# Optimization experiments

Hardware: AMD Instinct MI355X
Metric: run time of the kernel (lower is better)

Reference implementation:

```python
import jax, jax.numpy as jnp
import numpy as np

N, E, IN, ED, H = 50000, 500000, 27, 12, 128
LAYERS = 3


def _bn(h, g, b):
    # BatchNorm1d, training-mode batch statistics, biased variance, eps=1e-5
    mu = h.mean(0)
    var = h.var(0)
    return (h - mu) * jax.lax.rsqrt(var + 1e-5) * g + b


def _layer(x, src, dst, ea, eps, eW, eb, W1, b1, g1, be1, W2, b2, ng, nb):
    # GINEConv: project edge_attr to node dim, message = relu(x_j + e), sum-aggregate
    e = ea @ eW + eb                                   # [E, in_dim]
    m = jax.nn.relu(x[src] + e)                        # [E, in_dim]
    agg = jax.ops.segment_sum(m, dst, num_segments=N)  # [N, in_dim]
    h = (1.0 + eps) * x + agg
    # conv MLP: Linear -> BN -> ReLU -> (Dropout eval=id) -> Linear
    h = jax.nn.relu(_bn(h @ W1 + b1, g1, be1))
    h = h @ W2 + b2
    # outer BatchNorm -> ReLU -> (Dropout eval=id)
    return jax.nn.relu(_bn(h, ng, nb))


def setup_inputs() -> dict:
    key = jax.random.key(0)
    ks = iter(jax.random.split(key, 64))
    d = {}
    d["x"] = jax.random.normal(next(ks), (N, IN), jnp.float32)
    d["edge_index"] = jax.random.randint(next(ks), (2, E), 0, N, jnp.int32)
    d["edge_attr"] = jax.random.normal(next(ks), (E, ED), jnp.float32)
    for i in range(LAYERS):
        ind = IN if i == 0 else H
        d[f"l{i}_eps"] = jnp.zeros((), jnp.float32)
        d[f"l{i}_eW"] = jax.random.normal(next(ks), (ED, ind), jnp.float32) * 0.1
        d[f"l{i}_eb"] = jnp.zeros((ind,), jnp.float32)
        d[f"l{i}_W1"] = jax.random.normal(next(ks), (ind, 2 * H), jnp.float32) * (1.0 / np.sqrt(ind))
        d[f"l{i}_b1"] = jnp.zeros((2 * H,), jnp.float32)
        d[f"l{i}_g1"] = jnp.ones((2 * H,), jnp.float32)
        d[f"l{i}_be1"] = jnp.zeros((2 * H,), jnp.float32)
        d[f"l{i}_W2"] = jax.random.normal(next(ks), (2 * H, H), jnp.float32) * (1.0 / np.sqrt(2 * H))
        d[f"l{i}_b2"] = jnp.zeros((H,), jnp.float32)
        d[f"l{i}_ng"] = jnp.ones((H,), jnp.float32)
        d[f"l{i}_nb"] = jnp.zeros((H,), jnp.float32)
    return d


def reference(x, edge_index, edge_attr,
              l0_eps, l0_eW, l0_eb, l0_W1, l0_b1, l0_g1, l0_be1, l0_W2, l0_b2, l0_ng, l0_nb,
              l1_eps, l1_eW, l1_eb, l1_W1, l1_b1, l1_g1, l1_be1, l1_W2, l1_b2, l1_ng, l1_nb,
              l2_eps, l2_eW, l2_eb, l2_W1, l2_b1, l2_g1, l2_be1, l2_W2, l2_b2, l2_ng, l2_nb):
    src, dst = edge_index[0], edge_index[1]
    P = [
        (l0_eps, l0_eW, l0_eb, l0_W1, l0_b1, l0_g1, l0_be1, l0_W2, l0_b2, l0_ng, l0_nb),
        (l1_eps, l1_eW, l1_eb, l1_W1, l1_b1, l1_g1, l1_be1, l1_W2, l1_b2, l1_ng, l1_nb),
        (l2_eps, l2_eW, l2_eb, l2_W1, l2_b1, l2_g1, l2_be1, l2_W2, l2_b2, l2_ng, l2_nb),
    ]
    h = x
    for i, p in enumerate(P):
        out = _layer(h, src, dst, edge_attr, *p)
        if 0 < i < LAYERS - 1 and out.shape == h.shape:
            h = h + 0.3 * out
        else:
            h = out
    return h
```

## Files before the change

### kernel.cpp

```cpp
#include <hip/hip_runtime.h>
#include <hip/hip_bf16.h>


typedef __attribute__((ext_vector_type(8))) short bf16x8;
typedef __attribute__((ext_vector_type(4))) float f32x4;

static inline int cdiv(int a, int b) { return (a + b - 1) / b; }

__device__ inline ushort f2bf(float f) {
    uint32_t u = __float_as_uint(f);
    return (ushort)((u + 0x7FFFu + ((u >> 16) & 1u)) >> 16);
}
__device__ inline float bf2f(ushort h) { return __uint_as_float(((uint32_t)h) << 16); }

__global__ __launch_bounds__(256) void histogram_dst(const int* __restrict__ dst,
                                                     int* __restrict__ deg, int E) {
    int i = blockIdx.x * blockDim.x + threadIdx.x;
    int stride = gridDim.x * blockDim.x;
    for (; i < E; i += stride) atomicAdd(&deg[dst[i]], 1);
}

__global__ __launch_bounds__(1024) void scan_deg(const int* __restrict__ deg,
                                                 int* __restrict__ rowptr, int N) {
    __shared__ int part[1024];
    int t = threadIdx.x;
    int chunk = (N + 1023) / 1024;
    int b = t * chunk;
    int e = b + chunk;
    if (b > N) b = N;
    if (e > N) e = N;
    int s = 0;
    for (int i = b; i < e; ++i) s += deg[i];
    part[t] = s;
    __syncthreads();
    for (int off = 1; off < 1024; off <<= 1) {
        int v = (t >= off) ? part[t - off] : 0;
        __syncthreads();
        part[t] += v;
        __syncthreads();
    }
    int base = (t == 0) ? 0 : part[t - 1];
    for (int i = b; i < e; ++i) {
        rowptr[i] = base;
        base += deg[i];
    }
    if (t == 1023) rowptr[N] = base;
}

__global__ __launch_bounds__(256) void scatter_edges(const int* __restrict__ dst,
                                                     int* __restrict__ cursor,
                                                     int* __restrict__ eid, int E) {
    int i = blockIdx.x * blockDim.x + threadIdx.x;
    int stride = gridDim.x * blockDim.x;
    for (; i < E; i += stride) {
        int pos = atomicAdd(&cursor[dst[i]], 1);
        eid[pos] = i;
    }
}

__global__ __launch_bounds__(256) void gather128(
    const int* __restrict__ rowptr, const int* __restrict__ eid, const int* __restrict__ src,
    const float* __restrict__ ea, const float* __restrict__ eW, const float* __restrict__ eb,
    const float* __restrict__ x, const float* __restrict__ epsp, float* __restrict__ agg, int N) {
    __shared__ __align__(16) float sW[12 * 128];
    __shared__ __align__(16) float sb[128];
    int tid = threadIdx.x;
    for (int i = tid; i < 12 * 128; i += 256) sW[i] = eW[i];
    if (tid < 128) sb[tid] = eb[tid];
    __syncthreads();

    float onePlusEps = 1.0f + *epsp;
    int lane = tid & 31;
    int n = blockIdx.x * 8 + (tid >> 5);
    if (n >= N) return;
    int beg = rowptr[n], end = rowptr[n + 1];
    int d0 = lane << 2;
    float4 bb = *(const float4*)&sb[d0];
    float4 acc = make_float4(0.f, 0.f, 0.f, 0.f);

    int i = beg;
    for (; i + 4 <= end; i += 4) {
        int e[4], s[4];
        float av[4];
        float4 xv[4], p[4];
#pragma unroll
        for (int j = 0; j < 4; ++j) e[j] = eid[i + j];
#pragma unroll
        for (int j = 0; j < 4; ++j) {
            s[j] = src[e[j]];
            av[j] = (lane < 12) ? ea[(size_t)e[j] * 12 + lane] : 0.0f;
        }
#pragma unroll
        for (int j = 0; j < 4; ++j) {
            xv[j] = *(const float4*)&x[(size_t)s[j] * 128 + d0];
            p[j] = bb;
        }
#pragma unroll
        for (int k = 0; k < 12; ++k) {
            float4 w = *(const float4*)&sW[k * 128 + d0];
#pragma unroll
            for (int j = 0; j < 4; ++j) {
                float a = __shfl(av[j], k, 32);
                p[j].x = fmaf(a, w.x, p[j].x);
                p[j].y = fmaf(a, w.y, p[j].y);
                p[j].z = fmaf(a, w.z, p[j].z);
                p[j].w = fmaf(a, w.w, p[j].w);
            }
        }
#pragma unroll
        for (int j = 0; j < 4; ++j) {
            acc.x += fmaxf(xv[j].x + p[j].x, 0.f);
            acc.y += fmaxf(xv[j].y + p[j].y, 0.f);
            acc.z += fmaxf(xv[j].z + p[j].z, 0.f);
            acc.w += fmaxf(xv[j].w + p[j].w, 0.f);
        }
    }
    for (; i < end; ++i) {
        int e = eid[i];
        int s = src[e];
        float av = (lane < 12) ? ea[(size_t)e * 12 + lane] : 0.0f;
        float4 p = bb;
#pragma unroll
        for (int k = 0; k < 12; ++k) {
            float ak = __shfl(av, k, 32);
            float4 w = *(const float4*)&sW[k * 128 + d0];
            p.x = fmaf(ak, w.x, p.x);
            p.y = fmaf(ak, w.y, p.y);
            p.z = fmaf(ak, w.z, p.z);
            p.w = fmaf(ak, w.w, p.w);
        }
        float4 xv = *(const float4*)&x[(size_t)s * 128 + d0];
        acc.x += fmaxf(xv.x + p.x, 0.f);
        acc.y += fmaxf(xv.y + p.y, 0.f);
        acc.z += fmaxf(xv.z + p.z, 0.f);
        acc.w += fmaxf(xv.w + p.w, 0.f);
    }
    float4 xn = *(const float4*)&x[(size_t)n * 128 + d0];
    float4 o;
    o.x = fmaf(onePlusEps, xn.x, acc.x);
    o.y = fmaf(onePlusEps, xn.y, acc.y);
    o.z = fmaf(onePlusEps, xn.z, acc.z);
    o.w = fmaf(onePlusEps, xn.w, acc.w);
    *(float4*)&agg[(size_t)n * 128 + d0] = o;
}

__global__ __launch_bounds__(256) void gather27(
    const int* __restrict__ rowptr, const int* __restrict__ eid, const int* __restrict__ src,
    const float* __restrict__ ea, const float* __restrict__ eW, const float* __restrict__ eb,
    const float* __restrict__ x, const float* __restrict__ epsp, float* __restrict__ agg, int N) {
    __shared__ __align__(16) float sW[12 * 28 + 4];
    __shared__ __align__(16) float sb[32];
    int tid = threadIdx.x;
    for (int i = tid; i < 12 * 28 + 4; i += 256) sW[i] = 0.0f;
    if (tid < 32) sb[tid] = 0.0f;
    __syncthreads();
    for (int i = tid; i < 12 * 27; i += 256) {
        int k = i / 27, d = i - k * 27;
        sW[k * 28 + d] = eW[i];
    }
    if (tid < 27) sb[tid] = eb[tid];
    __syncthreads();

    float onePlusEps = 1.0f + *epsp;
    int lane = tid & 31;
    int n = blockIdx.x * 8 + (tid >> 5);
    if (n >= N) return;
    int beg = rowptr[n], end = rowptr[n + 1];
    int sub = lane >> 3, sl = lane & 7;
    int d0 = sl << 2;
    int d0c = (sl < 7) ? d0 : 24;
    float4 bb = *(const float4*)&sb[d0c];
    float4 acc = make_float4(0.f, 0.f, 0.f, 0.f);

    int iters = (end - beg + 3) >> 2;
    for (int it = 0; it < iters; ++it) {
        int i = beg + it * 4 + sub;
        bool v = i < end;
        int e = v ? eid[i] : 0;
        int s = v ? src[e] : 0;
        float avA = v ? ea[(size_t)e * 12 + sl] : 0.0f;
        float avB = (v && sl < 4) ? ea[(size_t)e * 12 + 8 + sl] : 0.0f;
        float4 xv = make_float4(0.f, 0.f, 0.f, 0.f);
        if (v) {
            if (sl < 6) {
                xv = *(const float4*)&x[(size_t)s * 27 + d0];
            } else if (sl == 6) {
                xv.x = x[(size_t)s * 27 + 24];
                xv.y = x[(size_t)s * 27 + 25];
                xv.z = x[(size_t)s * 27 + 26];
            }
        }
        float4 p = bb;
#pragma unroll
        for (int k = 0; k < 8; ++k) {
            float ak = __shfl(avA, k, 8);
            float4 w = *(const float4*)&sW[k * 28 + d0c];
            p.x = fmaf(ak, w.x, p.x);
            p.y = fmaf(ak, w.y, p.y);
            p.z = fmaf(ak, w.z, p.z);
            p.w = fmaf(ak, w.w, p.w);
        }
#pragma unroll
        for (int k = 8; k < 12; ++k) {
            float ak = __shfl(avB, k - 8, 8);
            float4 w = *(const float4*)&sW[k * 28 + d0c];
            p.x = fmaf(ak, w.x, p.x);
            p.y = fmaf(ak, w.y, p.y);
            p.z = fmaf(ak, w.z, p.z);
            p.w = fmaf(ak, w.w, p.w);
        }
        if (v) {
            acc.x += fmaxf(xv.x + p.x, 0.f);
            acc.y += fmaxf(xv.y + p.y, 0.f);
            acc.z += fmaxf(xv.z + p.z, 0.f);
            acc.w += fmaxf(xv.w + p.w, 0.f);
        }
    }
    acc.x += __shfl_xor(acc.x, 8, 32);
    acc.y += __shfl_xor(acc.y, 8, 32);
    acc.z += __shfl_xor(acc.z, 8, 32);
    acc.w += __shfl_xor(acc.w, 8, 32);
    acc.x += __shfl_xor(acc.x, 16, 32);
    acc.y += __shfl_xor(acc.y, 16, 32);
    acc.z += __shfl_xor(acc.z, 16, 32);
    acc.w += __shfl_xor(acc.w, 16, 32);

    if (sub == 0) {
        if (sl < 6) {
            float4 xn = *(const float4*)&x[(size_t)n * 27 + d0];
            float4 o;
            o.x = fmaf(onePlusEps, xn.x, acc.x);
            o.y = fmaf(onePlusEps, xn.y, acc.y);
            o.z = fmaf(onePlusEps, xn.z, acc.z);
            o.w = fmaf(onePlusEps, xn.w, acc.w);
            *(float4*)&agg[(size_t)n * 27 + d0] = o;
        } else if (sl == 6) {
            agg[(size_t)n * 27 + 24] = fmaf(onePlusEps, x[(size_t)n * 27 + 24], acc.x);
            agg[(size_t)n * 27 + 25] = fmaf(onePlusEps, x[(size_t)n * 27 + 25], acc.y);
            agg[(size_t)n * 27 + 26] = fmaf(onePlusEps, x[(size_t)n * 27 + 26], acc.z);
        }
    }
}

__global__ __launch_bounds__(256) void repack_w(const float* __restrict__ W, int K, int N,
                                                ushort* __restrict__ hi, ushort* __restrict__ lo) {
    int kg = (K + 31) / 32;
    int total = (N / 16) * kg * 64;
    int idx = blockIdx.x * 256 + threadIdx.x;
    if (idx >= total) return;
    int l = idx & 63;
    int g = (idx >> 6) % kg;
    int t = (idx >> 6) / kg;
#pragma unroll
    for (int j = 0; j < 8; ++j) {
        int k = g * 32 + ((l >> 4) << 3) + j;
        int n = (t << 4) + (l & 15);
        float v = (k < K) ? W[(size_t)k * N + n] : 0.0f;
        ushort h = f2bf(v);
        hi[(size_t)idx * 8 + j] = h;
        lo[(size_t)idx * 8 + j] = f2bf(v - bf2f(h));
    }
}

template <int NF, bool PRE_BN>
__global__ __launch_bounds__(512) void mfma_gemm(const float* __restrict__ A, int M, int K,
                                                 const ushort* __restrict__ Wph,
                                                 const ushort* __restrict__ Wpl,
                                                 const float* __restrict__ bias,
                                                 const float* __restrict__ scale,
                                                 const float* __restrict__ shift,
                                                 float* __restrict__ C, int ldc,
                                                 float* __restrict__ sums,
                                                 float* __restrict__ sumsq) {
    __shared__ __align__(16) ushort As_hi[128 * 32];
    __shared__ __align__(16) ushort As_lo[128 * 32];
    int tid = threadIdx.x;
    int lane = tid & 63;
    int wv = tid >> 6;
    int wm = wv >> 2, wn = wv & 3;
    int row0 = blockIdx.x * 128;
    int kg = (K + 31) >> 5;

    f32x4 acc[4][NF] = {};

    for (int g = 0; g < kg; ++g) {
        int k0 = g << 5;
        for (int c = tid; c < 1024; c += 512) {
            int row = c >> 3;
            int kc = (c & 7) << 2;
            int gm = row0 + row;
            float v[4] = {0.f, 0.f, 0.f, 0.f};
            if (gm < M) {
                const float* ap = &A[(size_t)gm * K + k0 + kc];
                if (k0 + kc + 4 <= K) {
                    float4 t4 = *(const float4*)ap;
                    v[0] = t4.x; v[1] = t4.y; v[2] = t4.z; v[3] = t4.w;
                } else {
#pragma unroll
                    for (int t = 0; t < 4; ++t)
                        if (k0 + kc + t < K) v[t] = ap[t];
                }
                if (PRE_BN) {
#pragma unroll
                    for (int t = 0; t < 4; ++t) {
                        int k = k0 + kc + t;
                        if (k < K) v[t] = fmaxf(fmaf(v[t], scale[k], shift[k]), 0.0f);
                    }
                }
            }
            ushort h[4], l2[4];
#pragma unroll
            for (int t = 0; t < 4; ++t) {
                h[t] = f2bf(v[t]);
                l2[t] = f2bf(v[t] - bf2f(h[t]));
            }
            int e = row * 32 + kc;
            *(ushort4*)&As_hi[e] = make_ushort4(h[0], h[1], h[2], h[3]);
            *(ushort4*)&As_lo[e] = make_ushort4(l2[0], l2[1], l2[2], l2[3]);
        }
        __syncthreads();

        bf16x8 ah[4], al[4];
#pragma unroll
        for (int mf = 0; mf < 4; ++mf) {
            int e = ((wm << 6) + (mf << 4) + (lane & 15)) * 32 + ((lane >> 4) << 3);
            ah[mf] = *(const bf16x8*)&As_hi[e];
            al[mf] = *(const bf16x8*)&As_lo[e];
        }
#pragma unroll
        for (int nf = 0; nf < NF; ++nf) {
            int tn = wn * NF + nf;
            size_t off = (((size_t)tn * kg + g) * 64 + lane) * 8;
            bf16x8 bh = *(const bf16x8*)(Wph + off);
            bf16x8 bl = *(const bf16x8*)(Wpl + off);
#pragma unroll
            for (int mf = 0; mf < 4; ++mf) {
                acc[mf][nf] =
                    __builtin_amdgcn_mfma_f32_16x16x32_bf16(ah[mf], bh, acc[mf][nf], 0, 0, 0);
                acc[mf][nf] =
                    __builtin_amdgcn_mfma_f32_16x16x32_bf16(ah[mf], bl, acc[mf][nf], 0, 0, 0);
                acc[mf][nf] =
                    __builtin_amdgcn_mfma_f32_16x16x32_bf16(al[mf], bh, acc[mf][nf], 0, 0, 0);
            }
        }
        __syncthreads();
    }

#pragma unroll
    for (int nf = 0; nf < NF; ++nf) {
        int col = (wn * NF + nf) * 16 + (lane & 15);
        float bv = bias[col];
        float s = 0.f, qs = 0.f;
#pragma unroll
        for (int mf = 0; mf < 4; ++mf) {
            int rbase = row0 + (wm << 6) + (mf << 4) + ((lane >> 4) << 2);
#pragma unroll
            for (int q = 0; q < 4; ++q) {
                int row = rbase + q;
                if (row < M) {
                    float v = acc[mf][nf][q] + bv;
                    C[(size_t)row * ldc + col] = v;
                    s += v;
                    qs = fmaf(v, v, qs);
                }
            }
        }
        s += __shfl_xor(s, 16);
        s += __shfl_xor(s, 32);
        qs += __shfl_xor(qs, 16);
        qs += __shfl_xor(qs, 32);
        if (lane < 16) {
            atomicAdd(&sums[col], s);
            atomicAdd(&sumsq[col], qs);
        }
    }
}

__global__ void finalize_bn(const float* __restrict__ sums, const float* __restrict__ sumsq,
                            const float* __restrict__ g, const float* __restrict__ b,
                            float* __restrict__ scale, float* __restrict__ shift, int C,
                            float invN) {
    int c = blockIdx.x * blockDim.x + threadIdx.x;
    if (c < C) {
        float mu = sums[c] * invN;
        float var = sumsq[c] * invN - mu * mu;
        float inv = rsqrtf(var + 1e-5f);
        float sc = g[c] * inv;
        scale[c] = sc;
        shift[c] = b[c] - mu * sc;
    }
}

template <bool RES>
__global__ __launch_bounds__(256) void bn_apply(const float* __restrict__ h,
                                                const float* __restrict__ scale,
                                                const float* __restrict__ shift,
                                                const float* __restrict__ xprev,
                                                float* __restrict__ out, int total4) {
    int i = blockIdx.x * blockDim.x + threadIdx.x;
    int stride = gridDim.x * blockDim.x;
    for (; i < total4; i += stride) {
        int c0 = (i & 31) << 2;
        float4 v = ((const float4*)h)[i];
        float4 o;
        o.x = fmaxf(fmaf(v.x, scale[c0 + 0], shift[c0 + 0]), 0.0f);
        o.y = fmaxf(fmaf(v.y, scale[c0 + 1], shift[c0 + 1]), 0.0f);
        o.z = fmaxf(fmaf(v.z, scale[c0 + 2], shift[c0 + 2]), 0.0f);
        o.w = fmaxf(fmaf(v.w, scale[c0 + 3], shift[c0 + 3]), 0.0f);
        if (RES) {
            float4 xp = ((const float4*)xprev)[i];
            o.x = fmaf(0.3f, o.x, xp.x);
            o.y = fmaf(0.3f, o.y, xp.y);
            o.z = fmaf(0.3f, o.z, xp.z);
            o.w = fmaf(0.3f, o.w, xp.w);
        }
        ((float4*)out)[i] = o;
    }
}

extern "C" void kernel_launch(void* const* d_in, const int* in_sizes, int n_in, void* d_out,
                              int out_size, void* d_ws, size_t ws_size, hipStream_t stream) {
    const float* x_in = (const float*)d_in[0];
    const int* ei = (const int*)d_in[1];
    const float* ea = (const float*)d_in[2];
    const int IN_DIM = 27;
    const int H = 128;
    int N = in_sizes[0] / IN_DIM;
    int E = in_sizes[1] / 2;
    const int* src = ei;
    const int* dst = ei + E;

    auto L = [&](int layer, int j) -> const float* {
        return (const float*)d_in[3 + 11 * layer + j];
    };

    float* X0 = (float*)d_ws;
    float* AGG = X0 + (size_t)N * H;
    float* H1 = AGG + (size_t)N * H;
    float* STATS = H1 + (size_t)N * 2 * H;
    float* sums1 = STATS;
    float* sq1 = STATS + 256;
    float* sums2 = STATS + 512;
    float* sq2 = STATS + 640;
    float* scale1 = STATS + 768;
    float* shift1 = STATS + 1024;
    float* scale2 = STATS + 1280;
    float* shift2 = STATS + 1408;
    int* rowptr = (int*)(STATS + 1536);
    int* cursor = rowptr + (N + 1);
    int* eid = cursor + N;
    size_t wp_off = ((size_t)(eid + E - (int*)d_ws) * 4 + 15) & ~(size_t)15;
    ushort* Wp1h = (ushort*)((char*)d_ws + wp_off);
    ushort* Wp1l = Wp1h + 32768;
    ushort* Wp2h = Wp1l + 32768;
    ushort* Wp2l = Wp2h + 32768;
    float* X1 = (float*)d_out;

    float invN = 1.0f / (float)N;
    int gridM = cdiv(N, 128);
    int gatherG = cdiv(N, 8);

    hipMemsetAsync(rowptr, 0, (size_t)(N + 1) * sizeof(int), stream);
    histogram_dst<<<1024, 256, 0, stream>>>(dst, rowptr, E);
    scan_deg<<<1, 1024, 0, stream>>>(rowptr, cursor, N);
    hipMemcpyAsync(rowptr, cursor, (size_t)(N + 1) * sizeof(int), hipMemcpyDeviceToDevice, stream);
    scatter_edges<<<1024, 256, 0, stream>>>(dst, cursor, eid, E);

    for (int i = 0; i < 3; ++i) {
        int ind = (i == 0) ? IN_DIM : H;
        const float* xin = (i == 0) ? x_in : ((i == 1) ? X0 : X1);
        float* xout = (i == 2) ? (float*)d_out : ((i == 0) ? X0 : X1);

        hipMemsetAsync(STATS, 0, 768 * sizeof(float), stream);

        int kg1 = cdiv(ind, 32);
        int tot1 = 16 * kg1 * 64;
        repack_w<<<cdiv(tot1, 256), 256, 0, stream>>>(L(i, 3), ind, 256, Wp1h, Wp1l);
        int tot2 = 8 * 8 * 64;
        repack_w<<<cdiv(tot2, 256), 256, 0, stream>>>(L(i, 7), 256, 128, Wp2h, Wp2l);

        if (i == 0)
            gather27<<<gatherG, 256, 0, stream>>>(rowptr, eid, src, ea, L(i, 1), L(i, 2), xin,
                                                  L(i, 0), AGG, N);
        else
            gather128<<<gatherG, 256, 0, stream>>>(rowptr, eid, src, ea, L(i, 1), L(i, 2), xin,
                                                   L(i, 0), AGG, N);

        mfma_gemm<4, false><<<gridM, 512, 0, stream>>>(AGG, N, ind, Wp1h, Wp1l, L(i, 4), nullptr,
                                                       nullptr, H1, 256, sums1, sq1);
        finalize_bn<<<1, 256, 0, stream>>>(sums1, sq1, L(i, 5), L(i, 6), scale1, shift1, 256, invN);

        mfma_gemm<2, true><<<gridM, 512, 0, stream>>>(H1, N, 256, Wp2h, Wp2l, L(i, 8), scale1,
                                                      shift1, AGG, 128, sums2, sq2);
        finalize_bn<<<1, 256, 0, stream>>>(sums2, sq2, L(i, 9), L(i, 10), scale2, shift2, 128,
                                           invN);

        int total4 = N * H / 4;
        if (i == 1)
            bn_apply<true><<<2048, 256, 0, stream>>>(AGG, scale2, shift2, X0, xout, total4);
        else
            bn_apply<false><<<2048, 256, 0, stream>>>(AGG, scale2, shift2, nullptr, xout, total4);
    }
}
```

Measured before the change: 821.1 us.

## Batch weight repacks, fold BN finalize into consumers, pad LDS, predicate gather tail

```diff
diff --git a/kernel.cpp b/kernel.cpp
--- a/kernel.cpp
+++ b/kernel.cpp
@@ -78,13 +78,17 @@
     float4 bb = *(const float4*)&sb[d0];
     float4 acc = make_float4(0.f, 0.f, 0.f, 0.f);
 
-    int i = beg;
-    for (; i + 4 <= end; i += 4) {
+    int iters = (end - beg + 3) >> 2;
+    for (int it = 0; it < iters; ++it) {
+        int i = beg + it * 4;
         int e[4], s[4];
         float av[4];
         float4 xv[4], p[4];
 #pragma unroll
-        for (int j = 0; j < 4; ++j) e[j] = eid[i + j];
+        for (int j = 0; j < 4; ++j) {
+            int idx = i + j;
+            e[j] = eid[(idx < end) ? idx : i];
+        }
 #pragma unroll
         for (int j = 0; j < 4; ++j) {
             s[j] = src[e[j]];
@@ -109,31 +113,12 @@
         }
 #pragma unroll
         for (int j = 0; j < 4; ++j) {
-            acc.x += fmaxf(xv[j].x + p[j].x, 0.f);
-            acc.y += fmaxf(xv[j].y + p[j].y, 0.f);
-            acc.z += fmaxf(xv[j].z + p[j].z, 0.f);
-            acc.w += fmaxf(xv[j].w + p[j].w, 0.f);
-        }
-    }
-    for (; i < end; ++i) {
-        int e = eid[i];
-        int s = src[e];
-        float av = (lane < 12) ? ea[(size_t)e * 12 + lane] : 0.0f;
-        float4 p = bb;
-#pragma unroll
-        for (int k = 0; k < 12; ++k) {
-            float ak = __shfl(av, k, 32);
-            float4 w = *(const float4*)&sW[k * 128 + d0];
-            p.x = fmaf(ak, w.x, p.x);
-            p.y = fmaf(ak, w.y, p.y);
-            p.z = fmaf(ak, w.z, p.z);
-            p.w = fmaf(ak, w.w, p.w);
-        }
-        float4 xv = *(const float4*)&x[(size_t)s * 128 + d0];
-        acc.x += fmaxf(xv.x + p.x, 0.f);
-        acc.y += fmaxf(xv.y + p.y, 0.f);
-        acc.z += fmaxf(xv.z + p.z, 0.f);
-        acc.w += fmaxf(xv.w + p.w, 0.f);
+            bool v = (i + j) < end;
+            acc.x += v ? fmaxf(xv[j].x + p[j].x, 0.f) : 0.f;
+            acc.y += v ? fmaxf(xv[j].y + p[j].y, 0.f) : 0.f;
+            acc.z += v ? fmaxf(xv[j].z + p[j].z, 0.f) : 0.f;
+            acc.w += v ? fmaxf(xv[j].w + p[j].w, 0.f) : 0.f;
+        }
     }
     float4 xn = *(const float4*)&x[(size_t)n * 128 + d0];
     float4 o;
@@ -242,20 +227,34 @@
     }
 }
 
-__global__ __launch_bounds__(256) void repack_w(const float* __restrict__ W, int K, int N,
-                                                ushort* __restrict__ hi, ushort* __restrict__ lo) {
-    int kg = (K + 31) / 32;
-    int total = (N / 16) * kg * 64;
+__global__ __launch_bounds__(256) void repack_all(const float* __restrict__ w0,
+                                                  const float* __restrict__ w1,
+                                                  const float* __restrict__ w2,
+                                                  const float* __restrict__ w3,
+                                                  const float* __restrict__ w4,
+                                                  const float* __restrict__ w5,
+                                                  ushort* __restrict__ hi,
+                                                  ushort* __restrict__ lo) {
     int idx = blockIdx.x * 256 + threadIdx.x;
-    if (idx >= total) return;
-    int l = idx & 63;
-    int g = (idx >> 6) % kg;
-    int t = (idx >> 6) / kg;
+    if (idx >= 21504) return;
+    const float* W;
+    int base, K, NC;
+    if (idx < 1024)       { W = w0; base = 0;     K = 27;  NC = 256; }
+    else if (idx < 5120)  { W = w1; base = 1024;  K = 256; NC = 128; }
+    else if (idx < 9216)  { W = w2; base = 5120;  K = 128; NC = 256; }
+    else if (idx < 13312) { W = w3; base = 9216;  K = 256; NC = 128; }
+    else if (idx < 17408) { W = w4; base = 13312; K = 128; NC = 256; }
+    else                  { W = w5; base = 17408; K = 256; NC = 128; }
+    int li = idx - base;
+    int kg = (K + 31) >> 5;
+    int l = li & 63;
+    int g = (li >> 6) % kg;
+    int t = (li >> 6) / kg;
 #pragma unroll
     for (int j = 0; j < 8; ++j) {
         int k = g * 32 + ((l >> 4) << 3) + j;
         int n = (t << 4) + (l & 15);
-        float v = (k < K) ? W[(size_t)k * N + n] : 0.0f;
+        float v = (k < K) ? W[(size_t)k * NC + n] : 0.0f;
         ushort h = f2bf(v);
         hi[(size_t)idx * 8 + j] = h;
         lo[(size_t)idx * 8 + j] = f2bf(v - bf2f(h));
@@ -263,23 +262,33 @@
 }
 
 template <int NF, bool PRE_BN>
-__global__ __launch_bounds__(512) void mfma_gemm(const float* __restrict__ A, int M, int K,
-                                                 const ushort* __restrict__ Wph,
-                                                 const ushort* __restrict__ Wpl,
-                                                 const float* __restrict__ bias,
-                                                 const float* __restrict__ scale,
-                                                 const float* __restrict__ shift,
-                                                 float* __restrict__ C, int ldc,
-                                                 float* __restrict__ sums,
-                                                 float* __restrict__ sumsq) {
-    __shared__ __align__(16) ushort As_hi[128 * 32];
-    __shared__ __align__(16) ushort As_lo[128 * 32];
+__global__ __launch_bounds__(512) void mfma_gemm(
+    const float* __restrict__ A, int M, int K, const ushort* __restrict__ Wph,
+    const ushort* __restrict__ Wpl, const float* __restrict__ bias,
+    const float* __restrict__ bn_sums, const float* __restrict__ bn_sq,
+    const float* __restrict__ bn_g, const float* __restrict__ bn_b, float invN,
+    float* __restrict__ C, int ldc, float* __restrict__ sums, float* __restrict__ sumsq) {
+    __shared__ __align__(16) ushort As_hi[128 * 40];
+    __shared__ __align__(16) ushort As_lo[128 * 40];
+    __shared__ float sSc[256], sSh[256];
     int tid = threadIdx.x;
     int lane = tid & 63;
     int wv = tid >> 6;
     int wm = wv >> 2, wn = wv & 3;
     int row0 = blockIdx.x * 128;
     int kg = (K + 31) >> 5;
+
+    if (PRE_BN) {
+        for (int k = tid; k < K; k += 512) {
+            float mu = bn_sums[k] * invN;
+            float var = bn_sq[k] * invN - mu * mu;
+            float inv = rsqrtf(var + 1e-5f);
+            float sc = bn_g[k] * inv;
+            sSc[k] = sc;
+            sSh[k] = bn_b[k] - mu * sc;
+        }
+        __syncthreads();
+    }
 
     f32x4 acc[4][NF] = {};
 
@@ -304,7 +313,7 @@
 #pragma unroll
                     for (int t = 0; t < 4; ++t) {
                         int k = k0 + kc + t;
-                        if (k < K) v[t] = fmaxf(fmaf(v[t], scale[k], shift[k]), 0.0f);
+                        if (k < K) v[t] = fmaxf(fmaf(v[t], sSc[k], sSh[k]), 0.0f);
                     }
                 }
             }
@@ -314,7 +323,7 @@
                 h[t] = f2bf(v[t]);
                 l2[t] = f2bf(v[t] - bf2f(h[t]));
             }
-            int e = row * 32 + kc;
+            int e = row * 40 + kc;
             *(ushort4*)&As_hi[e] = make_ushort4(h[0], h[1], h[2], h[3]);
             *(ushort4*)&As_lo[e] = make_ushort4(l2[0], l2[1], l2[2], l2[3]);
         }
@@ -323,7 +332,7 @@
         bf16x8 ah[4], al[4];
 #pragma unroll
         for (int mf = 0; mf < 4; ++mf) {
-            int e = ((wm << 6) + (mf << 4) + (lane & 15)) * 32 + ((lane >> 4) << 3);
+            int e = ((wm << 6) + (mf << 4) + (lane & 15)) * 40 + ((lane >> 4) << 3);
             ah[mf] = *(const bf16x8*)&As_hi[e];
             al[mf] = *(const bf16x8*)&As_lo[e];
         }
@@ -376,37 +385,35 @@
     }
 }
 
-__global__ void finalize_bn(const float* __restrict__ sums, const float* __restrict__ sumsq,
-                            const float* __restrict__ g, const float* __restrict__ b,
-                            float* __restrict__ scale, float* __restrict__ shift, int C,
-                            float invN) {
-    int c = blockIdx.x * blockDim.x + threadIdx.x;
-    if (c < C) {
-        float mu = sums[c] * invN;
-        float var = sumsq[c] * invN - mu * mu;
-        float inv = rsqrtf(var + 1e-5f);
-        float sc = g[c] * inv;
-        scale[c] = sc;
-        shift[c] = b[c] - mu * sc;
-    }
-}
-
 template <bool RES>
 __global__ __launch_bounds__(256) void bn_apply(const float* __restrict__ h,
-                                                const float* __restrict__ scale,
-                                                const float* __restrict__ shift,
+                                                const float* __restrict__ sums,
+                                                const float* __restrict__ sq,
+                                                const float* __restrict__ g,
+                                                const float* __restrict__ b, float invN,
                                                 const float* __restrict__ xprev,
                                                 float* __restrict__ out, int total4) {
-    int i = blockIdx.x * blockDim.x + threadIdx.x;
+    __shared__ float sSc[128], sSh[128];
+    int tid = threadIdx.x;
+    if (tid < 128) {
+        float mu = sums[tid] * invN;
+        float var = sq[tid] * invN - mu * mu;
+        float inv = rsqrtf(var + 1e-5f);
+        float sc = g[tid] * inv;
+        sSc[tid] = sc;
+        sSh[tid] = b[tid] - mu * sc;
+    }
+    __syncthreads();
+    int i = blockIdx.x * blockDim.x + tid;
     int stride = gridDim.x * blockDim.x;
     for (; i < total4; i += stride) {
         int c0 = (i & 31) << 2;
         float4 v = ((const float4*)h)[i];
         float4 o;
-        o.x = fmaxf(fmaf(v.x, scale[c0 + 0], shift[c0 + 0]), 0.0f);
-        o.y = fmaxf(fmaf(v.y, scale[c0 + 1], shift[c0 + 1]), 0.0f);
-        o.z = fmaxf(fmaf(v.z, scale[c0 + 2], shift[c0 + 2]), 0.0f);
-        o.w = fmaxf(fmaf(v.w, scale[c0 + 3], shift[c0 + 3]), 0.0f);
+        o.x = fmaxf(fmaf(v.x, sSc[c0 + 0], sSh[c0 + 0]), 0.0f);
+        o.y = fmaxf(fmaf(v.y, sSc[c0 + 1], sSh[c0 + 1]), 0.0f);
+        o.z = fmaxf(fmaf(v.z, sSc[c0 + 2], sSh[c0 + 2]), 0.0f);
+        o.w = fmaxf(fmaf(v.w, sSc[c0 + 3], sSh[c0 + 3]), 0.0f);
         if (RES) {
             float4 xp = ((const float4*)xprev)[i];
             o.x = fmaf(0.3f, o.x, xp.x);
@@ -438,30 +445,26 @@
     float* AGG = X0 + (size_t)N * H;
     float* H1 = AGG + (size_t)N * H;
     float* STATS = H1 + (size_t)N * 2 * H;
-    float* sums1 = STATS;
-    float* sq1 = STATS + 256;
-    float* sums2 = STATS + 512;
-    float* sq2 = STATS + 640;
-    float* scale1 = STATS + 768;
-    float* shift1 = STATS + 1024;
-    float* scale2 = STATS + 1280;
-    float* shift2 = STATS + 1408;
-    int* rowptr = (int*)(STATS + 1536);
+    int* rowptr = (int*)(STATS + 3 * 768);
     int* cursor = rowptr + (N + 1);
     int* eid = cursor + N;
     size_t wp_off = ((size_t)(eid + E - (int*)d_ws) * 4 + 15) & ~(size_t)15;
-    ushort* Wp1h = (ushort*)((char*)d_ws + wp_off);
-    ushort* Wp1l = Wp1h + 32768;
-    ushort* Wp2h = Wp1l + 32768;
-    ushort* Wp2l = Wp2h + 32768;
+    ushort* WpH = (ushort*)((char*)d_ws + wp_off);
+    ushort* WpL = WpH + (size_t)21504 * 8;
     float* X1 = (float*)d_out;
+
+    const size_t cum1[3] = {0, 5120, 13312};
+    const size_t cum2[3] = {1024, 9216, 17408};
 
     float invN = 1.0f / (float)N;
     int gridM = cdiv(N, 128);
     int gatherG = cdiv(N, 8);
 
     hipMemsetAsync(rowptr, 0, (size_t)(N + 1) * sizeof(int), stream);
+    hipMemsetAsync(STATS, 0, 3 * 768 * sizeof(float), stream);
     histogram_dst<<<1024, 256, 0, stream>>>(dst, rowptr, E);
+    repack_all<<<cdiv(21504, 256), 256, 0, stream>>>(L(0, 3), L(0, 7), L(1, 3), L(1, 7), L(2, 3),
+                                                     L(2, 7), WpH, WpL);
     scan_deg<<<1, 1024, 0, stream>>>(rowptr, cursor, N);
     hipMemcpyAsync(rowptr, cursor, (size_t)(N + 1) * sizeof(int), hipMemcpyDeviceToDevice, stream);
     scatter_edges<<<1024, 256, 0, stream>>>(dst, cursor, eid, E);
@@ -470,14 +473,10 @@
         int ind = (i == 0) ? IN_DIM : H;
         const float* xin = (i == 0) ? x_in : ((i == 1) ? X0 : X1);
         float* xout = (i == 2) ? (float*)d_out : ((i == 0) ? X0 : X1);
-
-        hipMemsetAsync(STATS, 0, 768 * sizeof(float), stream);
-
-        int kg1 = cdiv(ind, 32);
-        int tot1 = 16 * kg1 * 64;
-        repack_w<<<cdiv(tot1, 256), 256, 0, stream>>>(L(i, 3), ind, 256, Wp1h, Wp1l);
-        int tot2 = 8 * 8 * 64;
-        repack_w<<<cdiv(tot2, 256), 256, 0, stream>>>(L(i, 7), 256, 128, Wp2h, Wp2l);
+        float* sums1 = STATS + i * 768;
+        float* sq1 = sums1 + 256;
+        float* sums2 = sums1 + 512;
+        float* sq2 = sums1 + 640;
 
         if (i == 0)
             gather27<<<gatherG, 256, 0, stream>>>(rowptr, eid, src, ea, L(i, 1), L(i, 2), xin,
@@ -486,19 +485,20 @@
             gather128<<<gatherG, 256, 0, stream>>>(rowptr, eid, src, ea, L(i, 1), L(i, 2), xin,
                                                    L(i, 0), AGG, N);
 
-        mfma_gemm<4, false><<<gridM, 512, 0, stream>>>(AGG, N, ind, Wp1h, Wp1l, L(i, 4), nullptr,
-                                                       nullptr, H1, 256, sums1, sq1);
-        finalize_bn<<<1, 256, 0, stream>>>(sums1, sq1, L(i, 5), L(i, 6), scale1, shift1, 256, invN);
-
-        mfma_gemm<2, true><<<gridM, 512, 0, stream>>>(H1, N, 256, Wp2h, Wp2l, L(i, 8), scale1,
-                                                      shift1, AGG, 128, sums2, sq2);
-        finalize_bn<<<1, 256, 0, stream>>>(sums2, sq2, L(i, 9), L(i, 10), scale2, shift2, 128,
-                                           invN);
+        mfma_gemm<4, false><<<gridM, 512, 0, stream>>>(
+            AGG, N, ind, WpH + cum1[i] * 8, WpL + cum1[i] * 8, L(i, 4), nullptr, nullptr, nullptr,
+            nullptr, invN, H1, 256, sums1, sq1);
+
+        mfma_gemm<2, true><<<gridM, 512, 0, stream>>>(
+            H1, N, 256, WpH + cum2[i] * 8, WpL + cum2[i] * 8, L(i, 8), sums1, sq1, L(i, 5),
+            L(i, 6), invN, AGG, 128, sums2, sq2);
 
         int total4 = N * H / 4;
         if (i == 1)
-            bn_apply<true><<<2048, 256, 0, stream>>>(AGG, scale2, shift2, X0, xout, total4);
+            bn_apply<true><<<2048, 256, 0, stream>>>(AGG, sums2, sq2, L(i, 9), L(i, 10), invN, X0,
+                                                     xout, total4);
         else
-            bn_apply<false><<<2048, 256, 0, stream>>>(AGG, scale2, shift2, nullptr, xout, total4);
-    }
-}
+            bn_apply<false><<<2048, 256, 0, stream>>>(AGG, sums2, sq2, L(i, 9), L(i, 10), invN,
+                                                      nullptr, xout, total4);
+    }
+}
```

Result: no change. 835.8 us (+1.8%).
